# Kernel tuning notes

Hardware: AMD Instinct MI355X
Metric: run time of the kernel (lower is better)

Reference implementation:

```python
import jax, jax.numpy as jnp
import numpy as np

B, NGRID, NOBS, NPER, NLAYER, NC = 8, 4096, 4096, 32, 32, 50
SIGMA_SQ = 1.0   # sigma=1.0 in __init__
EPS = 1e-30
GRAD_CLIP = 1000.0


def setup_inputs() -> dict:
    key = jax.random.key(0)
    k1, k2, k3, k4, k5 = jax.random.split(key, 5)
    A = jax.random.uniform(k1, (NOBS, NGRID), dtype=jnp.float32)
    A = A / A.sum(axis=1, keepdims=True)  # row-normalized path matrix -> c_pred stays in velocity range
    c_true = 2.0 + 3.0 * jax.random.uniform(k2, (B, NGRID, NPER), dtype=jnp.float32)  # km/s, in-range of c_axis
    J = 0.1 * jax.random.normal(k3, (B, NGRID, NPER, NLAYER), dtype=jnp.float32)  # finite-diff dc/dVs Jacobians
    E_obs = jax.random.uniform(k4, (NOBS, NC, NPER), dtype=jnp.float32)  # beamforming energy spectra (c-axis downsampled to 50)
    c_axis = jnp.sort(1.5 + 4.0 * jax.random.uniform(k5, (NOBS, NC), dtype=jnp.float32), axis=1)
    return {"A": A, "c_true": c_true, "J": J, "E_obs": E_obs, "c_axis": c_axis}


def _solver3d(A, c_true, J, E_obs, c_axis):
    # --- logZ normalization, as computed in __init__ (trapezoidal integral over c_axis) ---
    emax = E_obs.max(axis=1)                                      # (O, P)
    integrand = jnp.exp(-(emax[:, None, :] - E_obs) / SIGMA_SQ)   # (O, Nc, P)
    dx = jnp.diff(c_axis, axis=1)                                 # (O, Nc-1)
    Z = jnp.sum(0.5 * (integrand[:, :-1] + integrand[:, 1:]) * dx[:, :, None], axis=1)
    logZ = jnp.log(Z + EPS)                                       # (O, P)

    # --- tomographic forward: slowness averaging along ray paths ---
    s_true = 1.0 / c_true                                         # (B, G, P)
    s_pred = jnp.einsum('og,bgp->bop', A, s_true)                 # (B, O, P)
    c_pred = 1.0 / s_pred

    # --- per-path linear interpolation of observed energy at predicted velocity ---
    idx = jax.vmap(jnp.searchsorted, in_axes=(0, 1), out_axes=1)(c_axis, c_pred)
    idx = jnp.clip(idx, 1, NC - 1)                                # (B, O, P)
    oi = jnp.arange(NOBS)[None, :, None]
    pi = jnp.arange(NPER)[None, None, :]
    x0 = c_axis[oi, idx - 1]
    x1 = c_axis[oi, idx]
    y0 = E_obs[oi, idx - 1, pi]
    y1 = E_obs[oi, idx, pi]
    t = (c_pred - x0) / (x1 - x0 + 1e-12)
    epred = y0 + t * (y1 - y0)
    dedc = (y1 - y0) / (x1 - x0 + 1e-12)
    log_num = -(emax[None] - epred) / SIGMA_SQ                    # (B, O, P)
    log_like = (log_num - logZ[None]).mean(axis=2).sum(axis=1)    # (B,) sum over paths of per-path mean

    # --- analytic chain-rule gradient w.r.t. Vs (as in solver3D_spec) ---
    dlogp_dc_pred = dedc / SIGMA_SQ                               # (B, O, P)
    dlogp_ds_pred = dlogp_dc_pred * (-1.0 / s_pred ** 2)
    dlogp_ds_true = jnp.einsum('og,bop->bgp', A, dlogp_ds_pred)   # A.T backprojection
    dlogp_dc_true = dlogp_ds_true * (-1.0 / c_true ** 2)          # (B, G, P)
    grad = jnp.einsum('bgpl,bgp->bgl', J, dlogp_dc_true)          # J[j].T @ dlogp_dc_true[j]
    grad = grad.reshape(grad.shape[0], -1)                        # (B, G*L)
    norm = jnp.linalg.norm(grad, axis=1, keepdims=True)
    grad = grad * jnp.where(norm > GRAD_CLIP, GRAD_CLIP / norm, 1.0)
    return log_like, grad


def reference(A, c_true, J, E_obs, c_axis):
    return _solver3d(A, c_true, J, E_obs, c_axis)
```

## Files before the change

### kernel.cpp

```cpp
#include <hip/hip_runtime.h>

#define kG 4096
#define kP 32
#define kL 32
#define kNC 50

typedef short bf16x8 __attribute__((ext_vector_type(8)));
typedef float f32x4 __attribute__((ext_vector_type(4)));
typedef unsigned short u16x4 __attribute__((ext_vector_type(4)));
typedef unsigned short u16x8 __attribute__((ext_vector_type(8)));

__device__ __forceinline__ unsigned short f2bf(float x) {
    unsigned u = __builtin_bit_cast(unsigned, x);
    u = (u + 0x7FFFu + ((u >> 16) & 1u)) >> 16;
    return (unsigned short)u;
}
__device__ __forceinline__ float bf2f(unsigned short b) {
    unsigned u = ((unsigned)b) << 16;
    return __builtin_bit_cast(float, u);
}

__global__ __launch_bounds__(256) void k_prep(const float* __restrict__ A,
        unsigned short* __restrict__ Ah, unsigned short* __restrict__ Al,
        unsigned short* __restrict__ AT) {
    __shared__ unsigned short tile[64][68];
    const int to = blockIdx.x >> 6, tg = blockIdx.x & 63;
    const int o0 = to << 6, g0 = tg << 6;
    const int tr = threadIdx.x >> 4;
    const int c4 = (threadIdx.x & 15) << 2;
    #pragma unroll
    for (int rr = tr; rr < 64; rr += 16) {
        float4 v = *(const float4*)(A + (size_t)(o0 + rr) * 4096 + g0 + c4);
        float vv[4] = {v.x, v.y, v.z, v.w};
        u16x4 h, l;
        #pragma unroll
        for (int q = 0; q < 4; ++q) {
            unsigned short hb = f2bf(vv[q]);
            h[q] = hb;
            l[q] = f2bf(vv[q] - bf2f(hb));
            tile[rr][c4 + q] = hb;
        }
        *(u16x4*)(Ah + (size_t)(o0 + rr) * 4096 + g0 + c4) = h;
        *(u16x4*)(Al + (size_t)(o0 + rr) * 4096 + g0 + c4) = l;
    }
    __syncthreads();
    #pragma unroll
    for (int rr = tr; rr < 64; rr += 16) {
        u16x4 tv;
        #pragma unroll
        for (int q = 0; q < 4; ++q) tv[q] = tile[c4 + q][rr];
        *(u16x4*)(AT + (size_t)(g0 + rr) * 4096 + o0 + c4) = tv;
    }
}

__global__ __launch_bounds__(256) void k_strue(const float* __restrict__ c_true,
        unsigned short* __restrict__ Sh, unsigned short* __restrict__ Sl) {
    __shared__ float sm[32][65];
    const int b = blockIdx.x >> 6;
    const int g0 = (blockIdx.x & 63) << 6;
    const int gl = threadIdx.x >> 5;
    const int p = threadIdx.x & 31;
    #pragma unroll
    for (int gg = gl; gg < 64; gg += 8) {
        float c = c_true[((size_t)(b << 12) + g0 + gg) * 32 + p];
        sm[p][gg] = 1.0f / c;
    }
    __syncthreads();
    const int p2 = threadIdx.x >> 3;
    const int gq = (threadIdx.x & 7) << 3;
    u16x8 h, l;
    #pragma unroll
    for (int q = 0; q < 8; ++q) {
        float s = sm[p2][gq + q];
        unsigned short hb = f2bf(s);
        h[q] = hb;
        l[q] = f2bf(s - bf2f(hb));
    }
    const size_t oidx = (size_t)(b * 32 + p2) * 4096 + g0 + gq;
    *(u16x8*)(Sh + oidx) = h;
    *(u16x8*)(Sl + oidx) = l;
}

__global__ __launch_bounds__(256) void k_emax(const float* __restrict__ E, const float* __restrict__ cax,
                       float* __restrict__ emax, float* __restrict__ logZ) {
    const int o = blockIdx.x * 8 + (threadIdx.x >> 5);
    const int p = threadIdx.x & 31;
    const float* e = E + (size_t)o * kNC * kP + p;
    float m = -1e30f;
    for (int c = 0; c < kNC; ++c) m = fmaxf(m, e[c * kP]);
    const float* ax = cax + o * kNC;
    float Z = 0.f;
    float prevI = __expf(e[0] - m);
    float prevx = ax[0];
    for (int c = 1; c < kNC; ++c) {
        float I = __expf(e[c * kP] - m);
        float x = ax[c];
        Z += 0.5f * (prevI + I) * (x - prevx);
        prevI = I; prevx = x;
    }
    emax[o * kP + p] = m;
    logZ[o * kP + p] = __logf(Z + 1e-30f);
}

template<int SPLIT>
__global__ __launch_bounds__(512, 4) void k_nt(const unsigned short* __restrict__ Ph,
        const unsigned short* __restrict__ Pl, const unsigned short* __restrict__ Qh,
        const unsigned short* __restrict__ Ql, float* __restrict__ outb) {
    const int kpart = blockIdx.x & 7;
    const int ct = blockIdx.x >> 3;
    const int c0 = ct << 6;
    const int wave = threadIdx.x >> 6;
    const int lane = threadIdx.x & 63;
    const int m0 = wave << 5;
    const int lrow = lane & 15;
    const int lk = (lane >> 4) << 3;
    const size_t koff = ((size_t)kpart << 9) + lk;

    const unsigned short* pah = Ph + (size_t)(m0 + lrow) * 4096 + koff;
    const unsigned short* pbh = Qh + (size_t)(c0 + lrow) * 4096 + koff;
    const unsigned short* pal = Pl + (size_t)(m0 + lrow) * 4096 + koff;
    const unsigned short* pbl = Ql + (size_t)(c0 + lrow) * 4096 + koff;

    f32x4 acc[2][4];
    #pragma unroll
    for (int i = 0; i < 2; ++i)
        #pragma unroll
        for (int j = 0; j < 4; ++j) acc[i][j] = (f32x4){0.f, 0.f, 0.f, 0.f};

    #pragma unroll 4
    for (int kk = 0; kk < 16; ++kk) {
        const int off = kk << 5;
        bf16x8 a0 = *(const bf16x8*)(pah + off);
        bf16x8 a1 = *(const bf16x8*)(pah + 16 * 4096 + off);
        bf16x8 b0 = *(const bf16x8*)(pbh + off);
        bf16x8 b1 = *(const bf16x8*)(pbh + 16 * 4096 + off);
        bf16x8 b2 = *(const bf16x8*)(pbh + 32 * 4096 + off);
        bf16x8 b3 = *(const bf16x8*)(pbh + 48 * 4096 + off);
        acc[0][0] = __builtin_amdgcn_mfma_f32_16x16x32_bf16(a0, b0, acc[0][0], 0, 0, 0);
        acc[0][1] = __builtin_amdgcn_mfma_f32_16x16x32_bf16(a0, b1, acc[0][1], 0, 0, 0);
        acc[0][2] = __builtin_amdgcn_mfma_f32_16x16x32_bf16(a0, b2, acc[0][2], 0, 0, 0);
        acc[0][3] = __builtin_amdgcn_mfma_f32_16x16x32_bf16(a0, b3, acc[0][3], 0, 0, 0);
        acc[1][0] = __builtin_amdgcn_mfma_f32_16x16x32_bf16(a1, b0, acc[1][0], 0, 0, 0);
        acc[1][1] = __builtin_amdgcn_mfma_f32_16x16x32_bf16(a1, b1, acc[1][1], 0, 0, 0);
        acc[1][2] = __builtin_amdgcn_mfma_f32_16x16x32_bf16(a1, b2, acc[1][2], 0, 0, 0);
        acc[1][3] = __builtin_amdgcn_mfma_f32_16x16x32_bf16(a1, b3, acc[1][3], 0, 0, 0);
        if (SPLIT) {
            bf16x8 a0l = *(const bf16x8*)(pal + off);
            bf16x8 a1l = *(const bf16x8*)(pal + 16 * 4096 + off);
            bf16x8 c0v = *(const bf16x8*)(pbl + off);
            bf16x8 c1v = *(const bf16x8*)(pbl + 16 * 4096 + off);
            bf16x8 c2v = *(const bf16x8*)(pbl + 32 * 4096 + off);
            bf16x8 c3v = *(const bf16x8*)(pbl + 48 * 4096 + off);
            acc[0][0] = __builtin_amdgcn_mfma_f32_16x16x32_bf16(a0l, b0, acc[0][0], 0, 0, 0);
            acc[0][1] = __builtin_amdgcn_mfma_f32_16x16x32_bf16(a0l, b1, acc[0][1], 0, 0, 0);
            acc[0][2] = __builtin_amdgcn_mfma_f32_16x16x32_bf16(a0l, b2, acc[0][2], 0, 0, 0);
            acc[0][3] = __builtin_amdgcn_mfma_f32_16x16x32_bf16(a0l, b3, acc[0][3], 0, 0, 0);
            acc[1][0] = __builtin_amdgcn_mfma_f32_16x16x32_bf16(a1l, b0, acc[1][0], 0, 0, 0);
            acc[1][1] = __builtin_amdgcn_mfma_f32_16x16x32_bf16(a1l, b1, acc[1][1], 0, 0, 0);
            acc[1][2] = __builtin_amdgcn_mfma_f32_16x16x32_bf16(a1l, b2, acc[1][2], 0, 0, 0);
            acc[1][3] = __builtin_amdgcn_mfma_f32_16x16x32_bf16(a1l, b3, acc[1][3], 0, 0, 0);
            acc[0][0] = __builtin_amdgcn_mfma_f32_16x16x32_bf16(a0, c0v, acc[0][0], 0, 0, 0);
            acc[0][1] = __builtin_amdgcn_mfma_f32_16x16x32_bf16(a0, c1v, acc[0][1], 0, 0, 0);
            acc[0][2] = __builtin_amdgcn_mfma_f32_16x16x32_bf16(a0, c2v, acc[0][2], 0, 0, 0);
            acc[0][3] = __builtin_amdgcn_mfma_f32_16x16x32_bf16(a0, c3v, acc[0][3], 0, 0, 0);
            acc[1][0] = __builtin_amdgcn_mfma_f32_16x16x32_bf16(a1, c0v, acc[1][0], 0, 0, 0);
            acc[1][1] = __builtin_amdgcn_mfma_f32_16x16x32_bf16(a1, c1v, acc[1][1], 0, 0, 0);
            acc[1][2] = __builtin_amdgcn_mfma_f32_16x16x32_bf16(a1, c2v, acc[1][2], 0, 0, 0);
            acc[1][3] = __builtin_amdgcn_mfma_f32_16x16x32_bf16(a1, c3v, acc[1][3], 0, 0, 0);
        }
    }

    float* out = outb + (size_t)kpart * (256 * 4096);
    const int rbase = (lane >> 4) << 2;
    #pragma unroll
    for (int i = 0; i < 2; ++i) {
        #pragma unroll
        for (int j = 0; j < 4; ++j) {
            const int col = c0 + j * 16 + lrow;
            #pragma unroll
            for (int q = 0; q < 4; ++q) {
                const int row = m0 + i * 16 + rbase + q;
                out[(size_t)row * 4096 + col] = acc[i][j][q];
            }
        }
    }
}

__global__ __launch_bounds__(256) void k_interp(const float* __restrict__ SP,
                         const float* __restrict__ E, const float* __restrict__ cax,
                         const float* __restrict__ emax, const float* __restrict__ logZ,
                         unsigned short* __restrict__ XT, float* __restrict__ loglike) {
    const int n = blockIdx.x >> 4;
    const int o = (blockIdx.x & 15) * 256 + threadIdx.x;
    const int b = n >> 5, p = n & 31;
    const size_t sidx = (size_t)n * 4096 + o;
    float s = 0.f;
    #pragma unroll
    for (int part = 0; part < 8; ++part) s += SP[sidx + (size_t)part * 1048576];
    float cp = 1.0f / s;
    const float* ax = cax + o * kNC;
    int lo = 0, hi = kNC;
    while (lo < hi) { int mid = (lo + hi) >> 1; if (ax[mid] < cp) lo = mid + 1; else hi = mid; }
    int bi = lo; if (bi < 1) bi = 1; if (bi > kNC - 1) bi = kNC - 1;
    float x0 = ax[bi - 1], x1 = ax[bi];
    float y0 = E[((size_t)o * kNC + bi - 1) * kP + p];
    float y1 = E[((size_t)o * kNC + bi) * kP + p];
    float invdx = 1.0f / (x1 - x0 + 1e-12f);
    float t = (cp - x0) * invdx;
    float epred = y0 + t * (y1 - y0);
    float dedc = (y1 - y0) * invdx;
    float term = (epred - emax[o * kP + p]) - logZ[o * kP + p];
    XT[sidx] = f2bf(-dedc * cp * cp);

    __shared__ float red[256];
    red[threadIdx.x] = term;
    __syncthreads();
    for (int st = 128; st > 0; st >>= 1) {
        if (threadIdx.x < st) red[threadIdx.x] += red[threadIdx.x + st];
        __syncthreads();
    }
    if (threadIdx.x == 0) atomicAdd(loglike + b, red[0] * (1.0f / 32.0f));
}

__global__ __launch_bounds__(256) void k_grad(const float* __restrict__ W, const float* __restrict__ c_true,
                       const float* __restrict__ J, float* __restrict__ gout,
                       float* __restrict__ normsq) {
    __shared__ float wsm[8][33];
    __shared__ float red[256];
    const int b = blockIdx.x >> 9;
    const int g0 = (blockIdx.x & 511) << 3;
    {
        const int p = threadIdx.x >> 3, gq = threadIdx.x & 7;
        const size_t widx = (size_t)(b * 32 + p) * 4096 + g0 + gq;
        float w = 0.f;
        #pragma unroll
        for (int part = 0; part < 8; ++part) w += W[widx + (size_t)part * 1048576];
        float ct = c_true[((size_t)(b << 12) + g0 + gq) * 32 + p];
        wsm[gq][p] = -w / (ct * ct);
    }
    __syncthreads();
    const int gq = threadIdx.x >> 5;
    const int l = threadIdx.x & 31;
    const int g = g0 + gq;
    const float* jrow = J + ((size_t)(b << 12) + g) * (kP * kL) + l;
    float acc = 0.f;
    #pragma unroll
    for (int p = 0; p < 32; ++p) acc += wsm[gq][p] * jrow[p * kL];
    gout[((size_t)(b << 12) + g) * kL + l] = acc;

    red[threadIdx.x] = acc * acc;
    __syncthreads();
    for (int st = 128; st > 0; st >>= 1) {
        if (threadIdx.x < st) red[threadIdx.x] += red[threadIdx.x + st];
        __syncthreads();
    }
    if (threadIdx.x == 0) atomicAdd(normsq + b, red[0]);
}

__global__ __launch_bounds__(256) void k_clip(float* __restrict__ gout, const float* __restrict__ normsq) {
    const int i = blockIdx.x * 256 + threadIdx.x;
    const int b = i >> 17;
    float norm = sqrtf(normsq[b]);
    float scale = norm > 1000.0f ? 1000.0f / norm : 1.0f;
    gout[i] *= scale;
}

extern "C" void kernel_launch(void* const* d_in, const int* in_sizes, int n_in,
                              void* d_out, int out_size, void* d_ws, size_t ws_size,
                              hipStream_t stream) {
    (void)in_sizes; (void)n_in; (void)out_size; (void)ws_size;
    const float* A      = (const float*)d_in[0];
    const float* c_true = (const float*)d_in[1];
    const float* J      = (const float*)d_in[2];
    const float* E_obs  = (const float*)d_in[3];
    const float* c_axis = (const float*)d_in[4];
    float* out = (float*)d_out;

    char* ws = (char*)d_ws;
    unsigned short* Ah   = (unsigned short*)(ws);
    unsigned short* Al   = (unsigned short*)(ws + 33554432);
    unsigned short* AT   = (unsigned short*)(ws + 67108864);
    unsigned short* Sh   = (unsigned short*)(ws + 100663296);
    unsigned short* Sl   = (unsigned short*)(ws + 102760448);
    unsigned short* XT   = (unsigned short*)(ws + 104857600);
    float* SP     = (float*)(ws + 106954752);
    float* Wb     = (float*)(ws + 140509184);
    float* emax   = (float*)(ws + 174063616);
    float* logZ   = (float*)(ws + 174587904);
    float* normsq = (float*)(ws + 175112192);

    hipMemsetAsync(out, 0, 8 * sizeof(float), stream);
    hipMemsetAsync(normsq, 0, 8 * sizeof(float), stream);

    k_prep<<<4096, 256, 0, stream>>>(A, Ah, Al, AT);
    k_strue<<<512, 256, 0, stream>>>(c_true, Sh, Sl);
    k_emax<<<512, 256, 0, stream>>>(E_obs, c_axis, emax, logZ);

    k_nt<1><<<512, 512, 0, stream>>>(Sh, Sl, Ah, Al, SP);

    k_interp<<<4096, 256, 0, stream>>>(SP, E_obs, c_axis, emax, logZ, XT, out);

    k_nt<0><<<512, 512, 0, stream>>>(XT, XT, AT, AT, Wb);

    k_grad<<<4096, 256, 0, stream>>>(Wb, c_true, J, out + 8, normsq);
    k_clip<<<4096, 256, 0, stream>>>(out + 8, normsq);
}
```

Measured before the change: 526.8 us.

## Rewrite GEMM kernel with LDS double-buffered 128x128 tiles and direct global-to-LDS loads

```diff
diff --git a/kernel.cpp b/kernel.cpp
--- a/kernel.cpp
+++ b/kernel.cpp
@@ -18,6 +18,12 @@
 __device__ __forceinline__ float bf2f(unsigned short b) {
     unsigned u = ((unsigned)b) << 16;
     return __builtin_bit_cast(float, u);
+}
+
+__device__ __forceinline__ void gload_lds16(const void* g, void* l) {
+    __builtin_amdgcn_global_load_lds(
+        (const __attribute__((address_space(1))) unsigned int*)g,
+        (__attribute__((address_space(3))) unsigned int*)l, 16, 0, 0);
 }
 
 __global__ __launch_bounds__(256) void k_prep(const float* __restrict__ A,
@@ -103,87 +109,128 @@
 }
 
 template<int SPLIT>
-__global__ __launch_bounds__(512, 4) void k_nt(const unsigned short* __restrict__ Ph,
+__global__ __launch_bounds__(512, 2) void k_nt2(const unsigned short* __restrict__ Ph,
         const unsigned short* __restrict__ Pl, const unsigned short* __restrict__ Qh,
         const unsigned short* __restrict__ Ql, float* __restrict__ outb) {
-    const int kpart = blockIdx.x & 7;
-    const int ct = blockIdx.x >> 3;
-    const int c0 = ct << 6;
-    const int wave = threadIdx.x >> 6;
-    const int lane = threadIdx.x & 63;
-    const int m0 = wave << 5;
+    constexpr int NTIL = SPLIT ? 4 : 2;
+    __shared__ __align__(16) unsigned short lds[2 * NTIL * 8192];
+
+    const int bid = blockIdx.x;
+    const int mt = bid & 1;
+    const int kp = (bid >> 1) & 3;
+    const int nt = bid >> 3;
+    const int mbase = mt << 7;
+    const int nbase = nt << 7;
+    const int kbase = kp << 10;
+
+    const int tid = threadIdx.x;
+    const int lane = tid & 63;
+    const int wid = tid >> 6;
+    const int wm = wid >> 2;
+    const int wn = wid & 3;
     const int lrow = lane & 15;
-    const int lk = (lane >> 4) << 3;
-    const size_t koff = ((size_t)kpart << 9) + lk;
-
-    const unsigned short* pah = Ph + (size_t)(m0 + lrow) * 4096 + koff;
-    const unsigned short* pbh = Qh + (size_t)(c0 + lrow) * 4096 + koff;
-    const unsigned short* pal = Pl + (size_t)(m0 + lrow) * 4096 + koff;
-    const unsigned short* pbl = Ql + (size_t)(c0 + lrow) * 4096 + koff;
-
-    f32x4 acc[2][4];
-    #pragma unroll
-    for (int i = 0; i < 2; ++i)
-        #pragma unroll
-        for (int j = 0; j < 4; ++j) acc[i][j] = (f32x4){0.f, 0.f, 0.f, 0.f};
-
-    #pragma unroll 4
-    for (int kk = 0; kk < 16; ++kk) {
-        const int off = kk << 5;
-        bf16x8 a0 = *(const bf16x8*)(pah + off);
-        bf16x8 a1 = *(const bf16x8*)(pah + 16 * 4096 + off);
-        bf16x8 b0 = *(const bf16x8*)(pbh + off);
-        bf16x8 b1 = *(const bf16x8*)(pbh + 16 * 4096 + off);
-        bf16x8 b2 = *(const bf16x8*)(pbh + 32 * 4096 + off);
-        bf16x8 b3 = *(const bf16x8*)(pbh + 48 * 4096 + off);
-        acc[0][0] = __builtin_amdgcn_mfma_f32_16x16x32_bf16(a0, b0, acc[0][0], 0, 0, 0);
-        acc[0][1] = __builtin_amdgcn_mfma_f32_16x16x32_bf16(a0, b1, acc[0][1], 0, 0, 0);
-        acc[0][2] = __builtin_amdgcn_mfma_f32_16x16x32_bf16(a0, b2, acc[0][2], 0, 0, 0);
-        acc[0][3] = __builtin_amdgcn_mfma_f32_16x16x32_bf16(a0, b3, acc[0][3], 0, 0, 0);
-        acc[1][0] = __builtin_amdgcn_mfma_f32_16x16x32_bf16(a1, b0, acc[1][0], 0, 0, 0);
-        acc[1][1] = __builtin_amdgcn_mfma_f32_16x16x32_bf16(a1, b1, acc[1][1], 0, 0, 0);
-        acc[1][2] = __builtin_amdgcn_mfma_f32_16x16x32_bf16(a1, b2, acc[1][2], 0, 0, 0);
-        acc[1][3] = __builtin_amdgcn_mfma_f32_16x16x32_bf16(a1, b3, acc[1][3], 0, 0, 0);
+    const int kg = lane >> 4;
+
+    int r_[2], ke_[2], Pb_[2];
+    #pragma unroll
+    for (int i = 0; i < 2; ++i) {
+        int P = (tid + (i << 9)) << 4;
+        int L = P ^ (((P >> 7) & 7) << 4);
+        Pb_[i] = P;
+        r_[i] = L >> 7;
+        ke_[i] = (L & 127) >> 1;
+    }
+
+    auto stage = [&](unsigned short* t, const unsigned short* src, int rb, int k0) {
+        #pragma unroll
+        for (int i = 0; i < 2; ++i) {
+            const unsigned short* g = src + (size_t)(rb + r_[i]) * 4096 + (k0 + ke_[i]);
+            gload_lds16(g, (char*)t + Pb_[i]);
+        }
+    };
+    auto stage_all = [&](int buf, int t) {
+        const int k0 = kbase + (t << 6);
+        unsigned short* base = lds + buf * (NTIL * 8192);
+        stage(base, Ph, mbase, k0);
+        stage(base + 8192, Qh, nbase, k0);
         if (SPLIT) {
-            bf16x8 a0l = *(const bf16x8*)(pal + off);
-            bf16x8 a1l = *(const bf16x8*)(pal + 16 * 4096 + off);
-            bf16x8 c0v = *(const bf16x8*)(pbl + off);
-            bf16x8 c1v = *(const bf16x8*)(pbl + 16 * 4096 + off);
-            bf16x8 c2v = *(const bf16x8*)(pbl + 32 * 4096 + off);
-            bf16x8 c3v = *(const bf16x8*)(pbl + 48 * 4096 + off);
-            acc[0][0] = __builtin_amdgcn_mfma_f32_16x16x32_bf16(a0l, b0, acc[0][0], 0, 0, 0);
-            acc[0][1] = __builtin_amdgcn_mfma_f32_16x16x32_bf16(a0l, b1, acc[0][1], 0, 0, 0);
-            acc[0][2] = __builtin_amdgcn_mfma_f32_16x16x32_bf16(a0l, b2, acc[0][2], 0, 0, 0);
-            acc[0][3] = __builtin_amdgcn_mfma_f32_16x16x32_bf16(a0l, b3, acc[0][3], 0, 0, 0);
-            acc[1][0] = __builtin_amdgcn_mfma_f32_16x16x32_bf16(a1l, b0, acc[1][0], 0, 0, 0);
-            acc[1][1] = __builtin_amdgcn_mfma_f32_16x16x32_bf16(a1l, b1, acc[1][1], 0, 0, 0);
-            acc[1][2] = __builtin_amdgcn_mfma_f32_16x16x32_bf16(a1l, b2, acc[1][2], 0, 0, 0);
-            acc[1][3] = __builtin_amdgcn_mfma_f32_16x16x32_bf16(a1l, b3, acc[1][3], 0, 0, 0);
-            acc[0][0] = __builtin_amdgcn_mfma_f32_16x16x32_bf16(a0, c0v, acc[0][0], 0, 0, 0);
-            acc[0][1] = __builtin_amdgcn_mfma_f32_16x16x32_bf16(a0, c1v, acc[0][1], 0, 0, 0);
-            acc[0][2] = __builtin_amdgcn_mfma_f32_16x16x32_bf16(a0, c2v, acc[0][2], 0, 0, 0);
-            acc[0][3] = __builtin_amdgcn_mfma_f32_16x16x32_bf16(a0, c3v, acc[0][3], 0, 0, 0);
-            acc[1][0] = __builtin_amdgcn_mfma_f32_16x16x32_bf16(a1, c0v, acc[1][0], 0, 0, 0);
-            acc[1][1] = __builtin_amdgcn_mfma_f32_16x16x32_bf16(a1, c1v, acc[1][1], 0, 0, 0);
-            acc[1][2] = __builtin_amdgcn_mfma_f32_16x16x32_bf16(a1, c2v, acc[1][2], 0, 0, 0);
-            acc[1][3] = __builtin_amdgcn_mfma_f32_16x16x32_bf16(a1, c3v, acc[1][3], 0, 0, 0);
-        }
-    }
-
-    float* out = outb + (size_t)kpart * (256 * 4096);
-    const int rbase = (lane >> 4) << 2;
-    #pragma unroll
-    for (int i = 0; i < 2; ++i) {
-        #pragma unroll
-        for (int j = 0; j < 4; ++j) {
-            const int col = c0 + j * 16 + lrow;
+            stage(base + 2 * 8192, Pl, mbase, k0);
+            stage(base + 3 * 8192, Ql, nbase, k0);
+        }
+    };
+    auto ldfrag = [&](const unsigned short* t, int r, int kc) -> bf16x8 {
+        int L = (r << 7) + (kc << 1);
+        int Pb = L ^ ((r & 7) << 4);
+        return *(const bf16x8*)((const char*)t + Pb);
+    };
+
+    f32x4 acc[4][2];
+    #pragma unroll
+    for (int fi = 0; fi < 4; ++fi)
+        #pragma unroll
+        for (int fj = 0; fj < 2; ++fj) acc[fi][fj] = (f32x4){0.f, 0.f, 0.f, 0.f};
+
+    auto compute = [&](int buf) {
+        const unsigned short* tb = lds + buf * (NTIL * 8192);
+        #pragma unroll
+        for (int kk = 0; kk < 2; ++kk) {
+            const int kc = (kk << 5) + (kg << 3);
+            bf16x8 ah[4], bh[2];
+            #pragma unroll
+            for (int fi = 0; fi < 4; ++fi)
+                ah[fi] = ldfrag(tb, (wm << 6) + (fi << 4) + lrow, kc);
+            #pragma unroll
+            for (int fj = 0; fj < 2; ++fj)
+                bh[fj] = ldfrag(tb + 8192, (wn << 5) + (fj << 4) + lrow, kc);
+            #pragma unroll
+            for (int fi = 0; fi < 4; ++fi)
+                #pragma unroll
+                for (int fj = 0; fj < 2; ++fj)
+                    acc[fi][fj] = __builtin_amdgcn_mfma_f32_16x16x32_bf16(ah[fi], bh[fj], acc[fi][fj], 0, 0, 0);
+            if (SPLIT) {
+                bf16x8 al[4], bl[2];
+                #pragma unroll
+                for (int fi = 0; fi < 4; ++fi)
+                    al[fi] = ldfrag(tb + 2 * 8192, (wm << 6) + (fi << 4) + lrow, kc);
+                #pragma unroll
+                for (int fj = 0; fj < 2; ++fj)
+                    bl[fj] = ldfrag(tb + 3 * 8192, (wn << 5) + (fj << 4) + lrow, kc);
+                #pragma unroll
+                for (int fi = 0; fi < 4; ++fi)
+                    #pragma unroll
+                    for (int fj = 0; fj < 2; ++fj) {
+                        acc[fi][fj] = __builtin_amdgcn_mfma_f32_16x16x32_bf16(al[fi], bh[fj], acc[fi][fj], 0, 0, 0);
+                        acc[fi][fj] = __builtin_amdgcn_mfma_f32_16x16x32_bf16(ah[fi], bl[fj], acc[fi][fj], 0, 0, 0);
+                    }
+            }
+        }
+    };
+
+    stage_all(0, 0);
+    __syncthreads();
+
+    int buf = 0;
+    #pragma unroll 1
+    for (int t = 0; t < 15; ++t) {
+        stage_all(buf ^ 1, t + 1);
+        compute(buf);
+        __syncthreads();
+        buf ^= 1;
+    }
+    compute(buf);
+
+    float* outp = outb + (size_t)kp * (256 * 4096);
+    #pragma unroll
+    for (int fi = 0; fi < 4; ++fi)
+        #pragma unroll
+        for (int fj = 0; fj < 2; ++fj) {
+            const int col = nbase + (wn << 5) + (fj << 4) + lrow;
             #pragma unroll
             for (int q = 0; q < 4; ++q) {
-                const int row = m0 + i * 16 + rbase + q;
-                out[(size_t)row * 4096 + col] = acc[i][j][q];
+                const int row = mbase + (wm << 6) + (fi << 4) + (kg << 2) + q;
+                outp[(size_t)row * 4096 + col] = acc[fi][fj][q];
             }
         }
-    }
 }
 
 __global__ __launch_bounds__(256) void k_interp(const float* __restrict__ SP,
@@ -196,7 +243,7 @@
     const size_t sidx = (size_t)n * 4096 + o;
     float s = 0.f;
     #pragma unroll
-    for (int part = 0; part < 8; ++part) s += SP[sidx + (size_t)part * 1048576];
+    for (int part = 0; part < 4; ++part) s += SP[sidx + (size_t)part * 1048576];
     float cp = 1.0f / s;
     const float* ax = cax + o * kNC;
     int lo = 0, hi = kNC;
@@ -234,7 +281,7 @@
         const size_t widx = (size_t)(b * 32 + p) * 4096 + g0 + gq;
         float w = 0.f;
         #pragma unroll
-        for (int part = 0; part < 8; ++part) w += W[widx + (size_t)part * 1048576];
+        for (int part = 0; part < 4; ++part) w += W[widx + (size_t)part * 1048576];
         float ct = c_true[((size_t)(b << 12) + g0 + gq) * 32 + p];
         wsm[gq][p] = -w / (ct * ct);
     }
@@ -296,11 +343,11 @@
     k_strue<<<512, 256, 0, stream>>>(c_true, Sh, Sl);
     k_emax<<<512, 256, 0, stream>>>(E_obs, c_axis, emax, logZ);
 
-    k_nt<1><<<512, 512, 0, stream>>>(Sh, Sl, Ah, Al, SP);
+    k_nt2<1><<<256, 512, 0, stream>>>(Sh, Sl, Ah, Al, SP);
 
     k_interp<<<4096, 256, 0, stream>>>(SP, E_obs, c_axis, emax, logZ, XT, out);
 
-    k_nt<0><<<512, 512, 0, stream>>>(XT, XT, AT, AT, Wb);
+    k_nt2<0><<<256, 512, 0, stream>>>(XT, XT, AT, AT, Wb);
 
     k_grad<<<4096, 256, 0, stream>>>(Wb, c_true, J, out + 8, normsq);
     k_clip<<<4096, 256, 0, stream>>>(out + 8, normsq);
```

Result: faster. 429.8 us (-18.4%).
